# Optimization experiments

Hardware: AMD Instinct MI355X
Metric: run time of the kernel (lower is better)

## Reference

```python
import jax, jax.numpy as jnp
import numpy as np
from collections import deque


def _build_graph_paths(N, E, seed=0):
    """Random directed graph; all-pairs BFS shortest paths (matches nx.shortest_path on
    the unweighted DiGraph). Returns flattened (pair_id, node_id) membership lists:
    for every reachable pair (i,j) and every node e on the shortest path i->j, one
    entry with pair_id=i*N+j, node_id=e. path_len[i*N+j] = number of nodes on the
    path (0 if unreachable)."""
    rng = np.random.default_rng(seed)
    src = rng.integers(0, N, E)
    dst = rng.integers(0, N, E)
    adj = [[] for _ in range(N)]
    for u, v in zip(src, dst):
        adj[u].append(int(v))
    pair_chunks, node_chunks = [], []
    path_len = np.zeros(N * N, dtype=np.int32)
    for s in range(N):
        dist = np.full(N, -1, np.int32)
        parent = np.full(N, -1, np.int32)
        dist[s] = 0
        parent[s] = s
        q = deque([s])
        while q:
            u = q.popleft()
            for v in adj[u]:
                if dist[v] < 0:
                    dist[v] = dist[u] + 1
                    parent[v] = u
                    q.append(v)
        reach = np.nonzero(dist >= 0)[0].astype(np.int32)
        path_len[s * N + reach] = dist[reach] + 1
        cur = reach.copy()
        rem = dist[reach].copy()          # steps remaining (records rem+1 nodes)
        pid = (s * N + reach).astype(np.int64)
        while cur.size:
            pair_chunks.append(pid.copy())
            node_chunks.append(cur.copy())
            m = rem > 0                   # keep walking toward the source
            cur = parent[cur[m]]
            rem = rem[m] - 1
            pid = pid[m]
    pair_id = np.concatenate(pair_chunks).astype(np.int32)
    node_id = np.concatenate(node_chunks).astype(np.int32)
    return pair_id, node_id, path_len


def setup_inputs() -> dict:
    N, DIM, H, E = 1024, 64, 16, 8192
    pair_id, node_id, path_len = _build_graph_paths(N, E, seed=0)
    key = jax.random.key(0)
    k1, k2, k3, k4 = jax.random.split(key, 4)
    x = jax.random.normal(k1, (N, DIM), jnp.float32)
    edge_attr = jax.random.normal(k2, (N, 4), jnp.float32)
    lim = 1.0 / np.sqrt(4.0)              # nn.Linear(4, H) default init range
    W = jax.random.uniform(k3, (H, 4), jnp.float32, -lim, lim)
    b = jax.random.uniform(k4, (H,), jnp.float32, -lim, lim)
    return {
        "x": x,
        "edge_attr": edge_attr,
        "W": W,
        "b": b,
        "pair_id": jnp.asarray(pair_id),
        "node_id": jnp.asarray(node_id),
        "path_len": jnp.asarray(path_len),
    }


def reference(x, edge_attr, W, b, pair_id, node_id, path_len):
    # Original: out[i,j] = mean_{e in shortest_path(i,j)} (W @ edge_attr[e] + b),
    # 0 where no path. Implemented as gather + segment_sum + one small GEMM
    # (exactly equal by linearity of the Linear layer).
    N = x.shape[0]
    H = W.shape[0]
    gathered = edge_attr[node_id]                                   # [P, 4]
    sums = jax.ops.segment_sum(gathered, pair_id, num_segments=N * N)  # [N*N, 4]
    L = path_len[:, None].astype(sums.dtype)                        # [N*N, 1]
    lin = sums @ W.T + L * b                                        # sum of per-node Linear outputs
    out = jnp.where(path_len[:, None] > 0, lin / jnp.maximum(L, 1.0), 0.0)
    out = out.reshape(N, N, H)
    return jnp.transpose(out, (2, 0, 1))                            # 'h w n -> n h w'
```

## Files before the change

kernel.cpp:

```cpp
#include <hip/hip_runtime.h>


#define BS 256
#define NW 4
#define KPT 4
#define NMAX 1024

typedef float f32x4 __attribute__((ext_vector_type(4)));
typedef int   i32x4 __attribute__((ext_vector_type(4)));

__global__ __launch_bounds__(BS) void ee_rowsum(
    const int* __restrict__ path_len, int* __restrict__ rowsum, int N)
{
    __shared__ int wred[NW];
    const int tid  = threadIdx.x;
    const int wave = tid >> 6;
    const int lane = tid & 63;
    const int s    = blockIdx.x;
    const i32x4 lv =
        *reinterpret_cast<const i32x4*>(path_len + (size_t)s * N + 4 * tid);
    int v = lv.x + lv.y + lv.z + lv.w;
    for (int o = 32; o > 0; o >>= 1) v += __shfl_down(v, o);
    if (lane == 0) wred[wave] = v;
    __syncthreads();
    if (tid == 0) rowsum[s] = wred[0] + wred[1] + wred[2] + wred[3];
}

__global__ __launch_bounds__(BS, 4) void ee_fused(
    const float* __restrict__ edge_attr,
    const float* __restrict__ W,
    const float* __restrict__ b,
    const int*   __restrict__ node_id,
    const int*   __restrict__ path_len,
    const int*   __restrict__ rowsum,
    float*       __restrict__ out,
    int N, int NN)
{
    __shared__ __align__(16) f32x4 psum[NMAX];
    __shared__ float sW[64];
    __shared__ float sbv[16];
    __shared__ int wcnt1[NW];
    __shared__ int wcnt0[NW];
    __shared__ int smaxw[NW];
    __shared__ int wlo[NW];

    const int tid   = threadIdx.x;
    const int wave  = tid >> 6;
    const int lane  = tid & 63;
    const int s     = blockIdx.x;
    const int sbase = s * N;

    if (tid < 64) sW[tid]  = W[tid];
    if (tid < 16) sbv[tid] = b[tid];

    f32x4 ea[KPT];
#pragma unroll
    for (int c = 0; c < KPT; ++c)
        ea[c] = *reinterpret_cast<const f32x4*>(edge_attr + 4 * (4 * tid + c));

    const i32x4 Lv = *reinterpret_cast<const i32x4*>(path_len + sbase + 4 * tid);
    int L[KPT] = { Lv.x, Lv.y, Lv.z, Lv.w };

    {
        const i32x4 rv = *reinterpret_cast<const i32x4*>(rowsum + 4 * tid);
        int part = 0;
#pragma unroll
        for (int c = 0; c < KPT; ++c)
            if (4 * tid + c < s) part += rv[c];
        for (int o = 32; o > 0; o >>= 1) part += __shfl_down(part, o);
        if (lane == 0) wlo[wave] = part;
    }

    unsigned long long b1[KPT];
    int wtot1 = 0, wtot0 = 0, m = 0;
#pragma unroll
    for (int c = 0; c < KPT; ++c) {
        b1[c] = __ballot(L[c] > 1);
        const unsigned long long b0 = __ballot(L[c] > 0);
        wtot1 += __popcll(b1[c]);
        wtot0 += __popcll(b0);
        m = max(m, L[c]);
    }
    for (int o = 32; o > 0; o >>= 1) m = max(m, __shfl_down(m, o));
    if (lane == 0) { wcnt1[wave] = wtot1; wcnt0[wave] = wtot0; smaxw[wave] = m; }
    __syncthreads();

    int n0 = 0, maxd = 0, prew = 0, lo = 0;
#pragma unroll
    for (int w = 0; w < NW; ++w) {
        n0  += wcnt0[w];
        maxd = max(maxd, smaxw[w]);
        lo  += wlo[w];
        if (w < wave) prew += wcnt1[w];
    }
    const unsigned long long below = (1ull << lane) - 1ull;
    int prelane = prew;
#pragma unroll
    for (int c = 0; c < KPT; ++c) prelane += __popcll(b1[c] & below);

    int par[KPT];
    {
        int prec = 0;
#pragma unroll
        for (int c = 0; c < KPT; ++c) {
            par[c] = 0;
            if (L[c] > 1)
                par[c] = node_id[lo + n0 + prelane + prec];
            prec += (L[c] > 1);
        }
    }

    f32x4 acc[KPT];
#pragma unroll
    for (int c = 0; c < KPT; ++c) acc[c] = (f32x4)0.f;

    for (int d = 0; d < maxd; ++d) {
#pragma unroll
        for (int c = 0; c < KPT; ++c) {
            if (L[c] == d + 1) {
                f32x4 e = ea[c];
                if (d) e += psum[par[c]];
                acc[c] = e;
                psum[4 * tid + c] = e;
            }
        }
        __syncthreads();
    }

    float fmul[KPT], gmul[KPT];
#pragma unroll
    for (int c = 0; c < KPT; ++c) {
        fmul[c] = (L[c] > 0) ? 1.0f / (float)L[c] : 0.0f;
        gmul[c] = (L[c] > 0) ? 1.0f : 0.0f;
    }
#pragma unroll
    for (int h = 0; h < 16; ++h) {
        const float w0 = sW[4 * h + 0], w1 = sW[4 * h + 1];
        const float w2 = sW[4 * h + 2], w3 = sW[4 * h + 3];
        const float bh = sbv[h];
        f32x4 v;
#pragma unroll
        for (int c = 0; c < KPT; ++c)
            v[c] = (acc[c].x * w0 + acc[c].y * w1 +
                    acc[c].z * w2 + acc[c].w * w3) * fmul[c] + bh * gmul[c];
        reinterpret_cast<f32x4*>(out + (size_t)h * NN + sbase)[tid] = v;
    }
}

extern "C" void kernel_launch(void* const* d_in, const int* in_sizes, int n_in,
                              void* d_out, int out_size, void* d_ws, size_t ws_size,
                              hipStream_t stream) {
    const float* edge_attr = (const float*)d_in[1];
    const float* W         = (const float*)d_in[2];
    const float* b         = (const float*)d_in[3];
    const int*   node_id   = (const int*)d_in[5];
    const int*   path_len  = (const int*)d_in[6];
    const int NN = in_sizes[6];
    const int N  = in_sizes[0] / 64;

    int* rowsum = (int*)d_ws;

    ee_rowsum<<<N, BS, 0, stream>>>(path_len, rowsum, N);
    ee_fused<<<N, BS, 0, stream>>>(edge_attr, W, b, node_id, path_len, rowsum,
                                   (float*)d_out, N, NN);
}
```

Baseline: 113.2 us.

## Assign one source row per wavefront to drop block-wide barriers

Restructures the fused kernel so each wavefront handles a whole source row (1024 targets, 16 per lane) instead of one block per row. Per-depth __syncthreads is replaced by a wave-local LDS wait, and reductions use wave shuffles instead of shared-memory cross-wave combining. Edge attributes are staged in LDS and each wave gets its own psum buffer, which raises LDS use to roughly 80KB per block and lowers occupancy. Each lane now also carries four times the registers and serial depth-loop work.

```diff
diff --git a/kernel.cpp b/kernel.cpp
--- a/kernel.cpp
+++ b/kernel.cpp
@@ -2,8 +2,6 @@
 
 
 #define BS 256
-#define NW 4
-#define KPT 4
 #define NMAX 1024
 
 typedef float f32x4 __attribute__((ext_vector_type(4)));
@@ -12,7 +10,7 @@
 __global__ __launch_bounds__(BS) void ee_rowsum(
     const int* __restrict__ path_len, int* __restrict__ rowsum, int N)
 {
-    __shared__ int wred[NW];
+    __shared__ int wred[4];
     const int tid  = threadIdx.x;
     const int wave = tid >> 6;
     const int lane = tid & 63;
@@ -26,7 +24,7 @@
     if (tid == 0) rowsum[s] = wred[0] + wred[1] + wred[2] + wred[3];
 }
 
-__global__ __launch_bounds__(BS, 4) void ee_fused(
+__global__ __launch_bounds__(BS) void ee_fused(
     const float* __restrict__ edge_attr,
     const float* __restrict__ W,
     const float* __restrict__ b,
@@ -36,114 +34,127 @@
     float*       __restrict__ out,
     int N, int NN)
 {
-    __shared__ __align__(16) f32x4 psum[NMAX];
+    __shared__ __align__(16) f32x4 sea[NMAX];
+    __shared__ __align__(16) f32x4 psum[4][NMAX];
     __shared__ float sW[64];
     __shared__ float sbv[16];
-    __shared__ int wcnt1[NW];
-    __shared__ int wcnt0[NW];
-    __shared__ int smaxw[NW];
-    __shared__ int wlo[NW];
 
-    const int tid   = threadIdx.x;
-    const int wave  = tid >> 6;
-    const int lane  = tid & 63;
-    const int s     = blockIdx.x;
-    const int sbase = s * N;
+    const int tid  = threadIdx.x;
+    const int wave = tid >> 6;
+    const int lane = tid & 63;
+    const int s    = blockIdx.x * 4 + wave;
+    const bool act = (s < N);
+    const int sbase = act ? s * N : 0;
 
+    for (int i = tid; i < N; i += BS)
+        sea[i] = *reinterpret_cast<const f32x4*>(edge_attr + 4 * i);
     if (tid < 64) sW[tid]  = W[tid];
     if (tid < 16) sbv[tid] = b[tid];
 
-    f32x4 ea[KPT];
+    int L[4][4];
+    unsigned long long b1[4][4];
+    int tot1[4];
+    int n0 = 0, maxd = 0, lo = 0;
+    int par[4][4];
+
+    if (act) {
+        i32x4 Lv[4], rv[4];
 #pragma unroll
-    for (int c = 0; c < KPT; ++c)
-        ea[c] = *reinterpret_cast<const f32x4*>(edge_attr + 4 * (4 * tid + c));
+        for (int g = 0; g < 4; ++g) {
+            const int j = g * 256 + 4 * lane;
+            Lv[g] = (j < N)
+                ? *reinterpret_cast<const i32x4*>(path_len + sbase + j)
+                : (i32x4)0;
+            rv[g] = (j < N)
+                ? *reinterpret_cast<const i32x4*>(rowsum + j)
+                : (i32x4)0;
+        }
+        int mypart = 0, mymax = 0;
+#pragma unroll
+        for (int g = 0; g < 4; ++g) {
+            tot1[g] = 0;
+#pragma unroll
+            for (int c = 0; c < 4; ++c) {
+                L[g][c] = Lv[g][c];
+                b1[g][c] = __ballot(L[g][c] > 1);
+                tot1[g] += __popcll(b1[g][c]);
+                n0 += __popcll(__ballot(L[g][c] > 0));
+                mymax = max(mymax, L[g][c]);
+                if (g * 256 + 4 * lane + c < s) mypart += rv[g][c];
+            }
+        }
+        for (int o = 1; o < 64; o <<= 1) {
+            mypart += __shfl_xor(mypart, o);
+            mymax   = max(mymax, __shfl_xor(mymax, o));
+        }
+        lo = mypart; maxd = mymax;
 
-    const i32x4 Lv = *reinterpret_cast<const i32x4*>(path_len + sbase + 4 * tid);
-    int L[KPT] = { Lv.x, Lv.y, Lv.z, Lv.w };
-
-    {
-        const i32x4 rv = *reinterpret_cast<const i32x4*>(rowsum + 4 * tid);
-        int part = 0;
+        const unsigned long long below = (1ull << lane) - 1ull;
 #pragma unroll
-        for (int c = 0; c < KPT; ++c)
-            if (4 * tid + c < s) part += rv[c];
-        for (int o = 32; o > 0; o >>= 1) part += __shfl_down(part, o);
-        if (lane == 0) wlo[wave] = part;
-    }
-
-    unsigned long long b1[KPT];
-    int wtot1 = 0, wtot0 = 0, m = 0;
+        for (int g = 0; g < 4; ++g) {
+            int preg = 0;
 #pragma unroll
-    for (int c = 0; c < KPT; ++c) {
-        b1[c] = __ballot(L[c] > 1);
-        const unsigned long long b0 = __ballot(L[c] > 0);
-        wtot1 += __popcll(b1[c]);
-        wtot0 += __popcll(b0);
-        m = max(m, L[c]);
-    }
-    for (int o = 32; o > 0; o >>= 1) m = max(m, __shfl_down(m, o));
-    if (lane == 0) { wcnt1[wave] = wtot1; wcnt0[wave] = wtot0; smaxw[wave] = m; }
-    __syncthreads();
-
-    int n0 = 0, maxd = 0, prew = 0, lo = 0;
+            for (int gp = 0; gp < 4; ++gp) if (gp < g) preg += tot1[gp];
+            int lanesum = 0;
 #pragma unroll
-    for (int w = 0; w < NW; ++w) {
-        n0  += wcnt0[w];
-        maxd = max(maxd, smaxw[w]);
-        lo  += wlo[w];
-        if (w < wave) prew += wcnt1[w];
-    }
-    const unsigned long long below = (1ull << lane) - 1ull;
-    int prelane = prew;
+            for (int c = 0; c < 4; ++c) lanesum += __popcll(b1[g][c] & below);
+            int prec = 0;
 #pragma unroll
-    for (int c = 0; c < KPT; ++c) prelane += __popcll(b1[c] & below);
-
-    int par[KPT];
-    {
-        int prec = 0;
-#pragma unroll
-        for (int c = 0; c < KPT; ++c) {
-            par[c] = 0;
-            if (L[c] > 1)
-                par[c] = node_id[lo + n0 + prelane + prec];
-            prec += (L[c] > 1);
+            for (int c = 0; c < 4; ++c) {
+                par[g][c] = 0;
+                if (L[g][c] > 1)
+                    par[g][c] = node_id[lo + n0 + preg + lanesum + prec];
+                prec += (L[g][c] > 1);
+            }
         }
     }
 
-    f32x4 acc[KPT];
-#pragma unroll
-    for (int c = 0; c < KPT; ++c) acc[c] = (f32x4)0.f;
+    __syncthreads();
 
+    if (!act) return;
+
+    f32x4* const psw = psum[wave];
     for (int d = 0; d < maxd; ++d) {
 #pragma unroll
-        for (int c = 0; c < KPT; ++c) {
-            if (L[c] == d + 1) {
-                f32x4 e = ea[c];
-                if (d) e += psum[par[c]];
-                acc[c] = e;
-                psum[4 * tid + c] = e;
+        for (int g = 0; g < 4; ++g)
+#pragma unroll
+            for (int c = 0; c < 4; ++c) {
+                if (L[g][c] == d + 1) {
+                    const int j = g * 256 + 4 * lane + c;
+                    f32x4 e = sea[j];
+                    if (d) e += psw[par[g][c]];
+                    psw[j] = e;
+                }
             }
-        }
-        __syncthreads();
+        asm volatile("s_waitcnt lgkmcnt(0)" ::: "memory");
+        __builtin_amdgcn_sched_barrier(0);
     }
 
-    float fmul[KPT], gmul[KPT];
 #pragma unroll
-    for (int c = 0; c < KPT; ++c) {
-        fmul[c] = (L[c] > 0) ? 1.0f / (float)L[c] : 0.0f;
-        gmul[c] = (L[c] > 0) ? 1.0f : 0.0f;
-    }
+    for (int g = 0; g < 4; ++g) {
+        const int jb = g * 256 + 4 * lane;
+        if (jb >= N) continue;
+        f32x4 p[4];
+        float fm[4];
 #pragma unroll
-    for (int h = 0; h < 16; ++h) {
-        const float w0 = sW[4 * h + 0], w1 = sW[4 * h + 1];
-        const float w2 = sW[4 * h + 2], w3 = sW[4 * h + 3];
-        const float bh = sbv[h];
-        f32x4 v;
+        for (int c = 0; c < 4; ++c) {
+            p[c]  = psw[jb + c];
+            fm[c] = (L[g][c] > 0) ? 1.0f / (float)L[g][c] : 0.0f;
+        }
 #pragma unroll
-        for (int c = 0; c < KPT; ++c)
-            v[c] = (acc[c].x * w0 + acc[c].y * w1 +
-                    acc[c].z * w2 + acc[c].w * w3) * fmul[c] + bh * gmul[c];
-        reinterpret_cast<f32x4*>(out + (size_t)h * NN + sbase)[tid] = v;
+        for (int h = 0; h < 16; ++h) {
+            const float w0 = sW[4 * h + 0], w1 = sW[4 * h + 1];
+            const float w2 = sW[4 * h + 2], w3 = sW[4 * h + 3];
+            const float bh = sbv[h];
+            f32x4 v;
+#pragma unroll
+            for (int c = 0; c < 4; ++c) {
+                const float dotc =
+                    p[c].x * w0 + p[c].y * w1 + p[c].z * w2 + p[c].w * w3;
+                v[c] = (L[g][c] > 0) ? dotc * fm[c] + bh : 0.0f;
+            }
+            *reinterpret_cast<f32x4*>(out + (size_t)h * NN + sbase + jb) = v;
+        }
     }
 }
 
@@ -161,6 +172,6 @@
     int* rowsum = (int*)d_ws;
 
     ee_rowsum<<<N, BS, 0, stream>>>(path_len, rowsum, N);
-    ee_fused<<<N, BS, 0, stream>>>(edge_attr, W, b, node_id, path_len, rowsum,
-                                   (float*)d_out, N, NN);
+    ee_fused<<<(N + 3) / 4, BS, 0, stream>>>(edge_attr, W, b, node_id, path_len,
+                                             rowsum, (float*)d_out, N, NN);
 }
```

Measured after the change: 117.5 us. 3.8% more time.

## Process four source rows per 1024-thread block with per-group shared buffers

Applied to the files above, without the earlier changes.

Each block of the fused kernel now handles four source nodes, with one 256-thread group per row and a separate shared-memory prefix buffer per group. The grid shrinks to a quarter and output stores cover four contiguous rows, aiming to amortize block setup and the W/b loads. In exchange, every group runs the depth loop to the block-wide maximum path depth, shared memory per block rises fourfold, and only one block lands per CU. The existing launch-bounds hint of four blocks per CU now applies to 1024-thread blocks, which may squeeze registers.

```diff
diff --git a/kernel.cpp b/kernel.cpp
--- a/kernel.cpp
+++ b/kernel.cpp
@@ -1,7 +1,8 @@
 #include <hip/hip_runtime.h>
 
 
-#define BS 256
+#define BS 1024
+#define NGRP 4
 #define NW 4
 #define KPT 4
 #define NMAX 1024
@@ -9,10 +10,10 @@
 typedef float f32x4 __attribute__((ext_vector_type(4)));
 typedef int   i32x4 __attribute__((ext_vector_type(4)));
 
-__global__ __launch_bounds__(BS) void ee_rowsum(
+__global__ __launch_bounds__(256) void ee_rowsum(
     const int* __restrict__ path_len, int* __restrict__ rowsum, int N)
 {
-    __shared__ int wred[NW];
+    __shared__ int wred[4];
     const int tid  = threadIdx.x;
     const int wave = tid >> 6;
     const int lane = tid & 63;
@@ -36,19 +37,22 @@
     float*       __restrict__ out,
     int N, int NN)
 {
-    __shared__ __align__(16) f32x4 psum[NMAX];
+    __shared__ __align__(16) f32x4 psum[NGRP][NMAX];
     __shared__ float sW[64];
     __shared__ float sbv[16];
-    __shared__ int wcnt1[NW];
-    __shared__ int wcnt0[NW];
-    __shared__ int smaxw[NW];
-    __shared__ int wlo[NW];
+    __shared__ int wcnt1[NGRP][NW];
+    __shared__ int wcnt0[NGRP][NW];
+    __shared__ int smaxw[NGRP][NW];
+    __shared__ int wlo  [NGRP][NW];
 
     const int tid   = threadIdx.x;
-    const int wave  = tid >> 6;
+    const int grp   = tid >> 8;
+    const int gtid  = tid & 255;
+    const int gwave = (tid >> 6) & 3;
     const int lane  = tid & 63;
-    const int s     = blockIdx.x;
-    const int sbase = s * N;
+    const int s     = blockIdx.x * NGRP + grp;
+    const bool act  = (s < N);
+    const int sbase = act ? s * N : 0;
 
     if (tid < 64) sW[tid]  = W[tid];
     if (tid < 16) sbv[tid] = b[tid];
@@ -56,19 +60,20 @@
     f32x4 ea[KPT];
 #pragma unroll
     for (int c = 0; c < KPT; ++c)
-        ea[c] = *reinterpret_cast<const f32x4*>(edge_attr + 4 * (4 * tid + c));
+        ea[c] = *reinterpret_cast<const f32x4*>(edge_attr + 4 * (4 * gtid + c));
 
-    const i32x4 Lv = *reinterpret_cast<const i32x4*>(path_len + sbase + 4 * tid);
+    i32x4 Lv = (i32x4)0;
+    if (act) Lv = *reinterpret_cast<const i32x4*>(path_len + sbase + 4 * gtid);
     int L[KPT] = { Lv.x, Lv.y, Lv.z, Lv.w };
 
     {
-        const i32x4 rv = *reinterpret_cast<const i32x4*>(rowsum + 4 * tid);
+        const i32x4 rv = *reinterpret_cast<const i32x4*>(rowsum + 4 * gtid);
         int part = 0;
 #pragma unroll
         for (int c = 0; c < KPT; ++c)
-            if (4 * tid + c < s) part += rv[c];
+            if (4 * gtid + c < s) part += rv[c];
         for (int o = 32; o > 0; o >>= 1) part += __shfl_down(part, o);
-        if (lane == 0) wlo[wave] = part;
+        if (lane == 0) wlo[grp][gwave] = part;
     }
 
     unsigned long long b1[KPT];
@@ -82,17 +87,26 @@
         m = max(m, L[c]);
     }
     for (int o = 32; o > 0; o >>= 1) m = max(m, __shfl_down(m, o));
-    if (lane == 0) { wcnt1[wave] = wtot1; wcnt0[wave] = wtot0; smaxw[wave] = m; }
+    if (lane == 0) {
+        wcnt1[grp][gwave] = wtot1;
+        wcnt0[grp][gwave] = wtot0;
+        smaxw[grp][gwave] = m;
+    }
     __syncthreads();
 
-    int n0 = 0, maxd = 0, prew = 0, lo = 0;
+    int n0 = 0, prew = 0, lo = 0;
 #pragma unroll
     for (int w = 0; w < NW; ++w) {
-        n0  += wcnt0[w];
-        maxd = max(maxd, smaxw[w]);
-        lo  += wlo[w];
-        if (w < wave) prew += wcnt1[w];
+        n0 += wcnt0[grp][w];
+        lo += wlo[grp][w];
+        if (w < gwave) prew += wcnt1[grp][w];
     }
+    int maxd = 0;
+#pragma unroll
+    for (int g = 0; g < NGRP; ++g)
+#pragma unroll
+        for (int w = 0; w < NW; ++w) maxd = max(maxd, smaxw[g][w]);
+
     const unsigned long long below = (1ull << lane) - 1ull;
     int prelane = prew;
 #pragma unroll
@@ -114,36 +128,40 @@
 #pragma unroll
     for (int c = 0; c < KPT; ++c) acc[c] = (f32x4)0.f;
 
+    f32x4* const psg = psum[grp];
     for (int d = 0; d < maxd; ++d) {
 #pragma unroll
         for (int c = 0; c < KPT; ++c) {
             if (L[c] == d + 1) {
                 f32x4 e = ea[c];
-                if (d) e += psum[par[c]];
+                if (d) e += psg[par[c]];
                 acc[c] = e;
-                psum[4 * tid + c] = e;
+                psg[4 * gtid + c] = e;
             }
         }
         __syncthreads();
     }
 
-    float fmul[KPT], gmul[KPT];
+    if (act) {
+        float fmul[KPT], gmul[KPT];
 #pragma unroll
-    for (int c = 0; c < KPT; ++c) {
-        fmul[c] = (L[c] > 0) ? 1.0f / (float)L[c] : 0.0f;
-        gmul[c] = (L[c] > 0) ? 1.0f : 0.0f;
-    }
+        for (int c = 0; c < KPT; ++c) {
+            fmul[c] = (L[c] > 0) ? 1.0f / (float)L[c] : 0.0f;
+            gmul[c] = (L[c] > 0) ? 1.0f : 0.0f;
+        }
+        const size_t obase = (size_t)blockIdx.x * NGRP * N;
 #pragma unroll
-    for (int h = 0; h < 16; ++h) {
-        const float w0 = sW[4 * h + 0], w1 = sW[4 * h + 1];
-        const float w2 = sW[4 * h + 2], w3 = sW[4 * h + 3];
-        const float bh = sbv[h];
-        f32x4 v;
+        for (int h = 0; h < 16; ++h) {
+            const float w0 = sW[4 * h + 0], w1 = sW[4 * h + 1];
+            const float w2 = sW[4 * h + 2], w3 = sW[4 * h + 3];
+            const float bh = sbv[h];
+            f32x4 v;
 #pragma unroll
-        for (int c = 0; c < KPT; ++c)
-            v[c] = (acc[c].x * w0 + acc[c].y * w1 +
-                    acc[c].z * w2 + acc[c].w * w3) * fmul[c] + bh * gmul[c];
-        reinterpret_cast<f32x4*>(out + (size_t)h * NN + sbase)[tid] = v;
+            for (int c = 0; c < KPT; ++c)
+                v[c] = (acc[c].x * w0 + acc[c].y * w1 +
+                        acc[c].z * w2 + acc[c].w * w3) * fmul[c] + bh * gmul[c];
+            reinterpret_cast<f32x4*>(out + (size_t)h * NN + obase)[tid] = v;
+        }
     }
 }
 
@@ -160,7 +178,7 @@
 
     int* rowsum = (int*)d_ws;
 
-    ee_rowsum<<<N, BS, 0, stream>>>(path_len, rowsum, N);
-    ee_fused<<<N, BS, 0, stream>>>(edge_attr, W, b, node_id, path_len, rowsum,
-                                   (float*)d_out, N, NN);
+    ee_rowsum<<<N, 256, 0, stream>>>(path_len, rowsum, N);
+    ee_fused<<<(N + NGRP - 1) / NGRP, BS, 0, stream>>>(
+        edge_attr, W, b, node_id, path_len, rowsum, (float*)d_out, N, NN);
 }
```

Result: slower. 115.8 us (+2.3%).
